# Optimization experiments

Measured on AMD Instinct MI355X. Metric: run time of the kernel, lower is better.

## Reference

```python
import jax
import jax.numpy as jnp
from jax import lax
import numpy as np

DIM = 1024
T = 2048
B = 16
N_GROUPS = 32
DELTA_INIT = -2.0


def _xavier(key, shape, gain=1.0):
    fan_in, fan_out = shape[1], shape[0]
    limit = gain * np.sqrt(6.0 / (fan_in + fan_out))
    return jax.random.uniform(key, shape, jnp.float32, -limit, limit)


def setup_inputs() -> dict:
    key = jax.random.key(0)
    k_x, k_wx, k_wd, k_wo = jax.random.split(key, 4)
    return {
        "x": jax.random.normal(k_x, (T, B, DIM), jnp.float32),
        "h0": jnp.zeros((B, DIM), jnp.float32),
        "W_x": _xavier(k_wx, (DIM, DIM)),
        "r_h": jnp.zeros((DIM,), jnp.float32),
        "b": jnp.zeros((DIM,), jnp.float32),
        "W_delta": _xavier(k_wd, (DIM, DIM), gain=0.1),
        "b_delta": jnp.full((DIM,), DELTA_INIT, jnp.float32),
        "W_out": _xavier(k_wo, (DIM, DIM)),
        "n_groups": N_GROUPS,
    }


def reference(x, h0, W_x, r_h, b, W_delta, b_delta, W_out, n_groups):
    Tn, Bn, D = x.shape
    gs = D // n_groups  # group_size
    # Precompute all input-dependent GEMMs in parallel over (T, B).
    delta = jax.nn.sigmoid(jnp.einsum('tbd,ed->tbe', x, W_delta) + b_delta)  # [T,B,D]
    cand_in = jnp.einsum('tbd,ed->tbe', x, W_x) + b                          # [T,B,D]

    def step(h_prev, inp):
        d_t, c_t = inp
        candidate = jnp.tanh(c_t + r_h * h_prev)           # diagonal recurrence
        h_new = (1.0 - d_t) * h_prev + d_t * candidate     # [B,D]
        compete = jax.nn.softmax(
            h_new.reshape(Bn, n_groups, gs), axis=-1).reshape(Bn, D)
        out = compete * jax.nn.silu(h_new @ W_out.T)
        return h_new, (h_new, out)

    _, (hs, outs) = lax.scan(step, h0, (delta, cand_in))
    h_all = jnp.concatenate([h0[None], hs], axis=0)  # [T+1,B,D]
    return h_all, outs
```

## Files before the change

### kernel.cpp

```cpp
#include <hip/hip_runtime.h>
#include <stdint.h>

#define DIMN 1024
#define TSTEPS 2048
#define BATCH 16
#define MTOT (TSTEPS*BATCH)
#define CH (BATCH*DIMN)

typedef unsigned short u16;
typedef __attribute__((ext_vector_type(8))) __bf16 bf16x8;
typedef __attribute__((ext_vector_type(4))) float floatx4;

__device__ __forceinline__ float bf2f(u16 u) {
    unsigned v = ((unsigned)u) << 16;
    return __builtin_bit_cast(float, v);
}
__device__ __forceinline__ u16 f2bf(float f) {
    __bf16 b = (__bf16)f;
    return __builtin_bit_cast(u16, b);
}
__device__ __forceinline__ void gl_lds16(const void* g, void* l) {
    __builtin_amdgcn_global_load_lds(
        (const __attribute__((address_space(1))) void*)g,
        (__attribute__((address_space(3))) void*)l,
        16, 0, 0);
}

#define LOG2E  1.4426950408889634f
#define LOG2E2 2.8853900817779268f

__global__ void cvt_kernel(const float* __restrict__ src, u16* __restrict__ dst, int n4) {
    int i = blockIdx.x * blockDim.x + threadIdx.x;
    if (i >= n4) return;
    float4 v = ((const float4*)src)[i];
    ushort4 o;
    o.x = f2bf(v.x); o.y = f2bf(v.y); o.z = f2bf(v.z); o.w = f2bf(v.w);
    ((ushort4*)dst)[i] = o;
}

__global__ __launch_bounds__(256) void gemm_bt(
    const u16* __restrict__ A, const u16* __restrict__ W,
    const float* __restrict__ bias,
    u16* __restrict__ outB, float* __restrict__ outF,
    const u16* __restrict__ cmp, int mode)
{
    __shared__ alignas(16) u16 a_sh[4][128 * 32];
    __shared__ alignas(16) u16 b_sh[4][128 * 32];
    const int tid  = threadIdx.x;
    const int lane = tid & 63;
    const int wave = tid >> 6;
    const int wm = wave & 1, wn = wave >> 1;
    const int fid = blockIdx.x;
    const int m0 = (fid & 255) * 128, n0 = (fid >> 8) * 128;
    const int row = lane & 15, quad = lane >> 4;

    const u16* Ag0 = A + (size_t)(m0 + (tid >> 2)) * DIMN + (tid & 3) * 8;
    const u16* Ag1 = Ag0 + (size_t)64 * DIMN;
    const u16* Wg0 = W + (size_t)(n0 + (tid >> 2)) * DIMN + (tid & 3) * 8;
    const u16* Wg1 = Wg0 + (size_t)64 * DIMN;

    floatx4 acc[4][4];
    #pragma unroll
    for (int i = 0; i < 4; i++)
        #pragma unroll
        for (int j = 0; j < 4; j++) acc[i][j] = (floatx4)(0.0f);

    int aoff[4], boff[4];
    #pragma unroll
    for (int i = 0; i < 4; i++) aoff[i] = (wm * 64 + i * 16 + row) * 32 + quad * 8;
    #pragma unroll
    for (int j = 0; j < 4; j++) boff[j] = (wn * 64 + j * 16 + row) * 32 + quad * 8;

    #define STAGE(t_) {                                                        \
        const int pb_ = (t_) & 3; const int kp_ = (t_) * 32;                   \
        gl_lds16(Ag0 + kp_, &a_sh[pb_][tid * 8]);                              \
        gl_lds16(Ag1 + kp_, &a_sh[pb_][2048 + tid * 8]);                       \
        gl_lds16(Wg0 + kp_, &b_sh[pb_][tid * 8]);                              \
        gl_lds16(Wg1 + kp_, &b_sh[pb_][2048 + tid * 8]);                       \
    }

    STAGE(0);
    STAGE(1);

    #pragma unroll
    for (int t = 0; t < 32; t++) {
        if (t + 2 < 32) STAGE(t + 2);
        if (t < 30)        { asm volatile("s_waitcnt vmcnt(8)" ::: "memory"); }
        else if (t == 30)  { asm volatile("s_waitcnt vmcnt(4)" ::: "memory"); }
        else               { asm volatile("s_waitcnt vmcnt(0)" ::: "memory"); }
        __builtin_amdgcn_sched_barrier(0);
        __builtin_amdgcn_s_barrier();
        const int buf = t & 3;
        bf16x8 av[4], bv[4];
        #pragma unroll
        for (int i = 0; i < 4; i++) av[i] = *(const bf16x8*)(&a_sh[buf][aoff[i]]);
        #pragma unroll
        for (int j = 0; j < 4; j++) bv[j] = *(const bf16x8*)(&b_sh[buf][boff[j]]);
        #pragma unroll
        for (int i = 0; i < 4; i++)
            #pragma unroll
            for (int j = 0; j < 4; j++)
                acc[i][j] = __builtin_amdgcn_mfma_f32_16x16x32_bf16(
                    av[i], bv[j], acc[i][j], 0, 0, 0);
    }
    #undef STAGE

    const int mb = m0 + wm * 64 + quad * 4;
    const int nb = n0 + wn * 64 + row;
    if (mode == 2) {
        #pragma unroll
        for (int i = 0; i < 4; i++)
            #pragma unroll
            for (int j = 0; j < 4; j++)
                #pragma unroll
                for (int r = 0; r < 4; r++) {
                    size_t idx = (size_t)(mb + i * 16 + r) * DIMN + (nb + j * 16);
                    float z = acc[i][j][r];
                    float sil = z * __builtin_amdgcn_rcpf(1.f + __builtin_amdgcn_exp2f(-z * LOG2E));
                    outF[idx] = bf2f(cmp[idx]) * sil;
                }
    } else if (mode == 0) {
        #pragma unroll
        for (int i = 0; i < 4; i++)
            #pragma unroll
            for (int j = 0; j < 4; j++)
                #pragma unroll
                for (int r = 0; r < 4; r++) {
                    int n = nb + j * 16;
                    float v = acc[i][j][r] + bias[n];
                    v = __builtin_amdgcn_rcpf(1.f + __builtin_amdgcn_exp2f(-v * LOG2E));
                    outB[(size_t)(mb + i * 16 + r) * DIMN + n] = f2bf(v);
                }
    } else {
        #pragma unroll
        for (int i = 0; i < 4; i++)
            #pragma unroll
            for (int j = 0; j < 4; j++)
                #pragma unroll
                for (int r = 0; r < 4; r++) {
                    int n = nb + j * 16;
                    float v = acc[i][j][r] + bias[n];
                    outB[(size_t)(mb + i * 16 + r) * DIMN + n] = f2bf(v);
                }
    }
}

#define CS 64
#define SB 8
__global__ __launch_bounds__(64) void scan_kernel(
    const u16* __restrict__ dB, const u16* __restrict__ cB,
    const float* __restrict__ h0, const float* __restrict__ r_h,
    float* __restrict__ hAll)
{
    __shared__ alignas(16) u16 d_sh[2][CS * 64];
    __shared__ alignas(16) u16 c_sh[2][CS * 64];
    const int tid = threadIdx.x;
    const int c0 = blockIdx.x * 64;
    const int c  = c0 + tid;
    const int d  = c & (DIMN - 1);

    float h = h0[c];
    const float r2 = r_h[d] * LOG2E2;
    hAll[c] = h;

    const u16* dG = dB + (size_t)(tid >> 3) * CH + c0 + (tid & 7) * 8;
    const u16* cG = cB + (size_t)(tid >> 3) * CH + c0 + (tid & 7) * 8;

    #pragma unroll
    for (int s = 0; s < 8; s++) {
        gl_lds16(dG + (size_t)(s * 8) * CH, (void*)&d_sh[0][s * 512]);
        gl_lds16(cG + (size_t)(s * 8) * CH, (void*)&c_sh[0][s * 512]);
    }

    float* hOut = hAll + CH + c;

    for (int t0 = 0; t0 < TSTEPS; t0 += CS) {
        const int buf = (t0 / CS) & 1;
        if (t0 + CS < TSTEPS) {
            #pragma unroll
            for (int s = 0; s < 8; s++) {
                gl_lds16(dG + (size_t)(t0 + CS + s * 8) * CH, (void*)&d_sh[buf ^ 1][s * 512]);
                gl_lds16(cG + (size_t)(t0 + CS + s * 8) * CH, (void*)&c_sh[buf ^ 1][s * 512]);
            }
        }
        if (t0 == 0) { asm volatile("s_waitcnt vmcnt(16)" ::: "memory"); }
        else         { asm volatile("s_waitcnt vmcnt(63)" ::: "memory"); }
        __builtin_amdgcn_sched_barrier(0);

        const u16* dS = d_sh[buf];
        const u16* cS = c_sh[buf];

        #pragma unroll
        for (int sb = 0; sb < CS / SB; sb++) {
            #pragma unroll
            for (int i = 0; i < SB; i++) {
                const int s = sb * SB + i;
                float dlt  = bf2f(dS[s * 64 + tid]);
                float cin2 = bf2f(cS[s * 64 + tid]) * LOG2E2;
                float e    = __builtin_amdgcn_exp2f(fmaf(r2, h, cin2));
                float q    = __builtin_amdgcn_rcpf(e + 1.f);
                float base = fmaf(-dlt, h, h) + dlt;
                float m2d  = -2.f * dlt;
                h = fmaf(m2d, q, base);
                hOut[(size_t)(t0 + s) * CH] = h;
            }
        }
    }
}

__global__ __launch_bounds__(256) void post_kernel(
    const float* __restrict__ hAll, u16* __restrict__ hB, u16* __restrict__ cmp)
{
    const int gid = blockIdx.x * 256 + threadIdx.x;
    float4 hv = ((const float4*)(hAll + CH))[gid];

    float ex = __builtin_amdgcn_exp2f(hv.x * LOG2E);
    float ey = __builtin_amdgcn_exp2f(hv.y * LOG2E);
    float ez = __builtin_amdgcn_exp2f(hv.z * LOG2E);
    float ew = __builtin_amdgcn_exp2f(hv.w * LOG2E);
    float sum = (ex + ey) + (ez + ew);
    #pragma unroll
    for (int s = 4; s > 0; s >>= 1) sum += __shfl_xor(sum, s);
    float inv = __builtin_amdgcn_rcpf(sum);

    ushort4 co, ho;
    co.x = f2bf(ex * inv); co.y = f2bf(ey * inv);
    co.z = f2bf(ez * inv); co.w = f2bf(ew * inv);
    ho.x = f2bf(hv.x); ho.y = f2bf(hv.y); ho.z = f2bf(hv.z); ho.w = f2bf(hv.w);
    ((ushort4*)cmp)[gid] = co;
    ((ushort4*)hB)[gid] = ho;
}

extern "C" void kernel_launch(void* const* d_in, const int* in_sizes, int n_in,
                              void* d_out, int out_size, void* d_ws, size_t ws_size,
                              hipStream_t stream) {
    const float* x   = (const float*)d_in[0];
    const float* h0  = (const float*)d_in[1];
    const float* W_x = (const float*)d_in[2];
    const float* r_h = (const float*)d_in[3];
    const float* b   = (const float*)d_in[4];
    const float* W_d = (const float*)d_in[5];
    const float* b_d = (const float*)d_in[6];
    const float* W_o = (const float*)d_in[7];
    float* out = (float*)d_out;

    char* ws = (char*)d_ws;
    u16* xb   = (u16*)(ws);
    u16* wdB  = (u16*)(ws + 67108864);
    u16* wxB  = (u16*)(ws + 69206016);
    u16* woB  = (u16*)(ws + 71303168);
    u16* dBuf = (u16*)(ws + 73400320);
    u16* cBuf = (u16*)(ws + 140509184);
    u16* cmpB = (u16*)(ws + 207618048);
    u16* hB   = xb;

    cvt_kernel<<<dim3(33554432 / 4 / 256), 256, 0, stream>>>(x, xb, 33554432 / 4);
    cvt_kernel<<<dim3(1048576 / 4 / 256), 256, 0, stream>>>(W_d, wdB, 1048576 / 4);
    cvt_kernel<<<dim3(1048576 / 4 / 256), 256, 0, stream>>>(W_x, wxB, 1048576 / 4);
    cvt_kernel<<<dim3(1048576 / 4 / 256), 256, 0, stream>>>(W_o, woB, 1048576 / 4);

    dim3 g(MTOT / 128 * (DIMN / 128));
    gemm_bt<<<g, 256, 0, stream>>>(xb, wdB, b_d, dBuf, nullptr, nullptr, 0);
    gemm_bt<<<g, 256, 0, stream>>>(xb, wxB, b,   cBuf, nullptr, nullptr, 1);
    scan_kernel<<<256, 64, 0, stream>>>(dBuf, cBuf, h0, r_h, out);
    post_kernel<<<dim3(TSTEPS * CH / 4 / 256), 256, 0, stream>>>(out, hB, cmpB);
    gemm_bt<<<g, 256, 0, stream>>>(hB, woB, nullptr, nullptr, out + 33570816, cmpB, 2);
}
```

Baseline: 808.7 us.

## Enlarge GEMM tiles to 256x256 with XOR-swizzled LDS and 512 threads

The bf16 GEMM now uses 256x256 output tiles with a K-step of 64 and 8 waves per block, each wave computing a 128x64 sub-tile. It switches from a 4-deep to a 2-deep LDS buffer and adds an XOR swizzle on the LDS layout to avoid bank conflicts. The aim is more data reuse per byte loaded and fewer LDS conflicts across the three GEMMs. The trade-offs are 128KB of LDS per block, a larger register footprint, shallower prefetch with a full vmcnt(0) wait every step, and only 512 blocks in the grid.

```diff
diff --git a/kernel.cpp b/kernel.cpp
--- a/kernel.cpp
+++ b/kernel.cpp
@@ -38,78 +38,90 @@
     ((ushort4*)dst)[i] = o;
 }
 
-__global__ __launch_bounds__(256) void gemm_bt(
+__global__ __launch_bounds__(512, 2) void gemm_bt(
     const u16* __restrict__ A, const u16* __restrict__ W,
     const float* __restrict__ bias,
     u16* __restrict__ outB, float* __restrict__ outF,
     const u16* __restrict__ cmp, int mode)
 {
-    __shared__ alignas(16) u16 a_sh[4][128 * 32];
-    __shared__ alignas(16) u16 b_sh[4][128 * 32];
+    __shared__ alignas(16) u16 a_sh[2][256 * 64];
+    __shared__ alignas(16) u16 b_sh[2][256 * 64];
     const int tid  = threadIdx.x;
     const int lane = tid & 63;
-    const int wave = tid >> 6;
-    const int wm = wave & 1, wn = wave >> 1;
+    const int wid  = tid >> 6;
+    const int wm = wid >> 2, wn = wid & 3;
     const int fid = blockIdx.x;
-    const int m0 = (fid & 255) * 128, n0 = (fid >> 8) * 128;
-    const int row = lane & 15, quad = lane >> 4;
-
-    const u16* Ag0 = A + (size_t)(m0 + (tid >> 2)) * DIMN + (tid & 3) * 8;
-    const u16* Ag1 = Ag0 + (size_t)64 * DIMN;
-    const u16* Wg0 = W + (size_t)(n0 + (tid >> 2)) * DIMN + (tid & 3) * 8;
-    const u16* Wg1 = Wg0 + (size_t)64 * DIMN;
-
-    floatx4 acc[4][4];
-    #pragma unroll
-    for (int i = 0; i < 4; i++)
+    const int m0 = (fid & 127) * 256, n0 = (fid >> 7) * 256;
+    const int row16 = lane & 15, quad = lane >> 4;
+    const int xm = (row16 & 7) << 4;
+
+    const u16* aSrc[4]; const u16* wSrc[4]; int dQ[4];
+    #pragma unroll
+    for (int l = 0; l < 4; l++) {
+        const int q = l * 512 + tid;
+        const int r = q >> 3;
+        const int cs = ((q & 7) ^ (r & 7)) * 8;
+        dQ[l] = q * 8;
+        aSrc[l] = A + (size_t)(m0 + r) * DIMN + cs;
+        wSrc[l] = W + (size_t)(n0 + r) * DIMN + cs;
+    }
+
+    floatx4 acc[8][4];
+    #pragma unroll
+    for (int i = 0; i < 8; i++)
         #pragma unroll
         for (int j = 0; j < 4; j++) acc[i][j] = (floatx4)(0.0f);
 
-    int aoff[4], boff[4];
-    #pragma unroll
-    for (int i = 0; i < 4; i++) aoff[i] = (wm * 64 + i * 16 + row) * 32 + quad * 8;
-    #pragma unroll
-    for (int j = 0; j < 4; j++) boff[j] = (wn * 64 + j * 16 + row) * 32 + quad * 8;
-
     #define STAGE(t_) {                                                        \
-        const int pb_ = (t_) & 3; const int kp_ = (t_) * 32;                   \
-        gl_lds16(Ag0 + kp_, &a_sh[pb_][tid * 8]);                              \
-        gl_lds16(Ag1 + kp_, &a_sh[pb_][2048 + tid * 8]);                       \
-        gl_lds16(Wg0 + kp_, &b_sh[pb_][tid * 8]);                              \
-        gl_lds16(Wg1 + kp_, &b_sh[pb_][2048 + tid * 8]);                       \
+        const int pb_ = (t_) & 1; const int kp_ = (t_) * 64;                   \
+        _Pragma("unroll")                                                      \
+        for (int l = 0; l < 4; l++) {                                          \
+            gl_lds16(aSrc[l] + kp_, &a_sh[pb_][dQ[l]]);                        \
+            gl_lds16(wSrc[l] + kp_, &b_sh[pb_][dQ[l]]);                        \
+        }                                                                      \
     }
 
     STAGE(0);
-    STAGE(1);
-
-    #pragma unroll
-    for (int t = 0; t < 32; t++) {
-        if (t + 2 < 32) STAGE(t + 2);
-        if (t < 30)        { asm volatile("s_waitcnt vmcnt(8)" ::: "memory"); }
-        else if (t == 30)  { asm volatile("s_waitcnt vmcnt(4)" ::: "memory"); }
-        else               { asm volatile("s_waitcnt vmcnt(0)" ::: "memory"); }
+    asm volatile("s_waitcnt vmcnt(0)" ::: "memory");
+    __builtin_amdgcn_sched_barrier(0);
+    __builtin_amdgcn_s_barrier();
+    __builtin_amdgcn_sched_barrier(0);
+
+    #pragma unroll
+    for (int t = 0; t < 16; t++) {
+        if (t < 15) STAGE(t + 1);
+        const char* ab = (const char*)a_sh[t & 1];
+        const char* bb = (const char*)b_sh[t & 1];
+        #pragma unroll
+        for (int ks = 0; ks < 2; ks++) {
+            bf16x8 av[8], bv[4];
+            #pragma unroll
+            for (int i = 0; i < 8; i++)
+                av[i] = *(const bf16x8*)(ab +
+                    (((wm * 128 + i * 16 + row16) * 128 + ks * 64 + quad * 16) ^ xm));
+            #pragma unroll
+            for (int j = 0; j < 4; j++)
+                bv[j] = *(const bf16x8*)(bb +
+                    (((wn * 64 + j * 16 + row16) * 128 + ks * 64 + quad * 16) ^ xm));
+            #pragma unroll
+            for (int i = 0; i < 8; i++)
+                #pragma unroll
+                for (int j = 0; j < 4; j++)
+                    acc[i][j] = __builtin_amdgcn_mfma_f32_16x16x32_bf16(
+                        av[i], bv[j], acc[i][j], 0, 0, 0);
+        }
+        asm volatile("s_waitcnt vmcnt(0)" ::: "memory");
         __builtin_amdgcn_sched_barrier(0);
         __builtin_amdgcn_s_barrier();
-        const int buf = t & 3;
-        bf16x8 av[4], bv[4];
-        #pragma unroll
-        for (int i = 0; i < 4; i++) av[i] = *(const bf16x8*)(&a_sh[buf][aoff[i]]);
-        #pragma unroll
-        for (int j = 0; j < 4; j++) bv[j] = *(const bf16x8*)(&b_sh[buf][boff[j]]);
-        #pragma unroll
-        for (int i = 0; i < 4; i++)
-            #pragma unroll
-            for (int j = 0; j < 4; j++)
-                acc[i][j] = __builtin_amdgcn_mfma_f32_16x16x32_bf16(
-                    av[i], bv[j], acc[i][j], 0, 0, 0);
+        __builtin_amdgcn_sched_barrier(0);
     }
     #undef STAGE
 
-    const int mb = m0 + wm * 64 + quad * 4;
-    const int nb = n0 + wn * 64 + row;
+    const int mb = m0 + wm * 128 + quad * 4;
+    const int nb = n0 + wn * 64 + row16;
     if (mode == 2) {
         #pragma unroll
-        for (int i = 0; i < 4; i++)
+        for (int i = 0; i < 8; i++)
             #pragma unroll
             for (int j = 0; j < 4; j++)
                 #pragma unroll
@@ -121,7 +133,7 @@
                 }
     } else if (mode == 0) {
         #pragma unroll
-        for (int i = 0; i < 4; i++)
+        for (int i = 0; i < 8; i++)
             #pragma unroll
             for (int j = 0; j < 4; j++)
                 #pragma unroll
@@ -133,7 +145,7 @@
                 }
     } else {
         #pragma unroll
-        for (int i = 0; i < 4; i++)
+        for (int i = 0; i < 8; i++)
             #pragma unroll
             for (int j = 0; j < 4; j++)
                 #pragma unroll
@@ -259,10 +271,10 @@
     cvt_kernel<<<dim3(1048576 / 4 / 256), 256, 0, stream>>>(W_x, wxB, 1048576 / 4);
     cvt_kernel<<<dim3(1048576 / 4 / 256), 256, 0, stream>>>(W_o, woB, 1048576 / 4);
 
-    dim3 g(MTOT / 128 * (DIMN / 128));
-    gemm_bt<<<g, 256, 0, stream>>>(xb, wdB, b_d, dBuf, nullptr, nullptr, 0);
-    gemm_bt<<<g, 256, 0, stream>>>(xb, wxB, b,   cBuf, nullptr, nullptr, 1);
+    dim3 g(MTOT / 256 * (DIMN / 256));
+    gemm_bt<<<g, 512, 0, stream>>>(xb, wdB, b_d, dBuf, nullptr, nullptr, 0);
+    gemm_bt<<<g, 512, 0, stream>>>(xb, wxB, b,   cBuf, nullptr, nullptr, 1);
     scan_kernel<<<256, 64, 0, stream>>>(dBuf, cBuf, h0, r_h, out);
     post_kernel<<<dim3(TSTEPS * CH / 4 / 256), 256, 0, stream>>>(out, hB, cmpB);
-    gemm_bt<<<g, 256, 0, stream>>>(hB, woB, nullptr, nullptr, out + 33570816, cmpB, 2);
-}
+    gemm_bt<<<g, 512, 0, stream>>>(hB, woB, nullptr, nullptr, out + 33570816, cmpB, 2);
+}
```

Result: faster. 780.8 us (-3.4%).
